# Optimization experiments

Hardware: AMD Instinct MI355X
Metric: run time of the kernel (lower is better)

The kernel has to match this reference:

```python
import jax, jax.numpy as jnp
import numpy as np

B, T, C, H = 8, 2048, 768, 64  # batch, seq_len, embedding_dim, head_size


def setup_inputs() -> dict:
    key = jax.random.key(0)
    k1, k2, k3, k4 = jax.random.split(key, 4)
    x = jax.random.normal(k1, (B, T, C), dtype=jnp.float32)
    attention_mask = jnp.ones((B, T), dtype=jnp.float32)
    # nn.Linear(C, H, bias=False) weights stored pre-transposed as (C, H)
    scale = 0.02
    Wq = jax.random.normal(k2, (C, H), dtype=jnp.float32) * scale
    Wk = jax.random.normal(k3, (C, H), dtype=jnp.float32) * scale
    Wv = jax.random.normal(k4, (C, H), dtype=jnp.float32) * scale
    return {"x": x, "attention_mask": attention_mask, "Wq": Wq, "Wk": Wk, "Wv": Wv}


def reference(x, attention_mask, Wq, Wk, Wv):
    # x: [B,T,C]; attention_mask: [B,T] (multiplied per query row)
    head_size = Wq.shape[-1]
    q = x @ Wq  # [B,T,H]
    k = x @ Wk  # [B,T,H]
    v = x @ Wv  # [B,T,H]
    inv_sqrt_h = jnp.asarray(1.0 / np.sqrt(head_size), x.dtype)
    s = jnp.einsum('bqh,bkh->bqk', q, k) * inv_sqrt_h  # [B,T,T]
    # attention_mask.unsqueeze(2) * qK ; masked_fill(qK == 0, -inf)
    s = attention_mask[:, :, None] * s
    s = jnp.where(s == 0, -jnp.inf, s)
    # causal tril mask
    seq = x.shape[1]
    tril = jnp.tril(jnp.ones((seq, seq), dtype=bool))
    s = jnp.where(tril[None, :, :], s, -jnp.inf)
    p = jax.nn.softmax(s, axis=-1)
    # dropout p=0.0 -> identity; nan cleanup (fully-masked rows)
    p = jnp.where(jnp.isnan(p), jnp.asarray(0.0, p.dtype), p)
    out = jnp.einsum('bqk,bkh->bqh', p, v)  # [B,T,H]
    return out
```

## Files before the change

### kernel.cpp

```cpp
#include <hip/hip_runtime.h>
#include <hip/hip_bf16.h>

#define B_ 8
#define T_ 2048
#define C_ 768
#define H_ 64
#define BT_ (B_*T_)

typedef __attribute__((ext_vector_type(8))) short bf16x8;
typedef __attribute__((ext_vector_type(4))) float f32x4;

__device__ __forceinline__ unsigned short f2bf(float x) {
    __hip_bfloat16 h = __float2bfloat16(x);
    return __builtin_bit_cast(unsigned short, h);
}

__device__ __forceinline__ bf16x8 cvt8(float4 a, float4 b) {
    bf16x8 r;
    r[0] = (short)f2bf(a.x); r[1] = (short)f2bf(a.y);
    r[2] = (short)f2bf(a.z); r[3] = (short)f2bf(a.w);
    r[4] = (short)f2bf(b.x); r[5] = (short)f2bf(b.y);
    r[6] = (short)f2bf(b.z); r[7] = (short)f2bf(b.w);
    return r;
}

__global__ __launch_bounds__(256) void wprep(
    const float* __restrict__ Wq, const float* __restrict__ Wk,
    const float* __restrict__ Wv, unsigned short* __restrict__ WTf)
{
    __shared__ float tile[32][68];
    const int bid = blockIdx.x;
    const int m = bid / 24, gc = bid % 24;
    const float* __restrict__ W = (m == 0) ? Wq : (m == 1) ? Wk : Wv;
    const int t = threadIdx.x;
    {
        const int r = t >> 3, c0 = (t & 7) * 8;
        float4 a = *(const float4*)(W + (size_t)(gc * 32 + r) * H_ + c0);
        float4 b = *(const float4*)(W + (size_t)(gc * 32 + r) * H_ + c0 + 4);
        *(float4*)&tile[r][c0]     = a;
        *(float4*)&tile[r][c0 + 4] = b;
    }
    __syncthreads();
    const int fl = t >> 6, lane = t & 63;
    const int q16 = lane & 15, quad = lane >> 4;
    const int f = m * 4 + fl;
    ushort4 u0, u1;
    u0.x = f2bf(tile[quad * 8 + 0][fl * 16 + q16]);
    u0.y = f2bf(tile[quad * 8 + 1][fl * 16 + q16]);
    u0.z = f2bf(tile[quad * 8 + 2][fl * 16 + q16]);
    u0.w = f2bf(tile[quad * 8 + 3][fl * 16 + q16]);
    u1.x = f2bf(tile[quad * 8 + 4][fl * 16 + q16]);
    u1.y = f2bf(tile[quad * 8 + 5][fl * 16 + q16]);
    u1.z = f2bf(tile[quad * 8 + 6][fl * 16 + q16]);
    u1.w = f2bf(tile[quad * 8 + 7][fl * 16 + q16]);
    unsigned short* __restrict__ dst = WTf + ((size_t)(gc * 12 + f) * 64 + lane) * 8;
    *(ushort4*)(dst)     = u0;
    *(ushort4*)(dst + 4) = u1;
}

__global__ __launch_bounds__(256, 4) void qkv_kernel(
    const float* __restrict__ x, const unsigned short* __restrict__ WTf,
    unsigned short* __restrict__ qF, unsigned short* __restrict__ kF,
    unsigned short* __restrict__ vF)
{
    __shared__ __align__(16) char shraw[3 * 64 * 49 * 4];
    unsigned short* xS = (unsigned short*)shraw;
    float (*mrg)[64][49] = (float (*)[64][49])shraw;

    const int tid  = threadIdx.x;
    const int w    = tid >> 6;
    const int lane = tid & 63;
    const int q16  = lane & 15, quad = lane >> 4;
    const int rowBase = blockIdx.x << 4;

    {
        const int r = tid >> 4, l = tid & 15;
        const float* __restrict__ xrow = x + (size_t)(rowBase + r) * C_;
        #pragma unroll
        for (int i = 0; i < 6; i++) {
            const int j = i * 16 + l;
            float4 a = *(const float4*)(xrow + j * 8);
            float4 b = *(const float4*)(xrow + j * 8 + 4);
            *(bf16x8*)&xS[(size_t)r * 772 + j * 8] = cvt8(a, b);
        }
    }
    __syncthreads();

    const unsigned short* __restrict__ xrowS = xS + q16 * 772 + w * 192 + quad * 8;
    f32x4 acc[12] = {};
    #pragma unroll
    for (int c = 0; c < 6; c++) {
        const int gc = w * 6 + c;
        const unsigned short* __restrict__ wpc = WTf + ((size_t)gc * 12) * 512 + lane * 8;
        bf16x8 xf = *(const bf16x8*)(xrowS + c * 32);
        bf16x8 wf[12];
        #pragma unroll
        for (int f = 0; f < 12; f++)
            wf[f] = *(const bf16x8*)(wpc + f * 512);
        #pragma unroll
        for (int f = 0; f < 12; f++)
            acc[f] = __builtin_amdgcn_mfma_f32_16x16x32_bf16(wf[f], xf, acc[f], 0, 0, 0);
    }
    __syncthreads();

    if (w > 0) {
        #pragma unroll
        for (int f = 0; f < 12; f++)
            #pragma unroll
            for (int r = 0; r < 4; r++) mrg[w - 1][lane][f * 4 + r] = acc[f][r];
    }
    __syncthreads();
    if (w == 0) {
        #pragma unroll
        for (int j = 0; j < 3; j++)
            #pragma unroll
            for (int f = 0; f < 12; f++)
                #pragma unroll
                for (int r = 0; r < 4; r++) acc[f][r] += mrg[j][lane][f * 4 + r];

        const size_t gt = (size_t)(rowBase >> 4);
        #pragma unroll
        for (int f = 0; f < 8; f++) {
            ushort4 u;
            u.x = f2bf(acc[f][0]); u.y = f2bf(acc[f][1]);
            u.z = f2bf(acc[f][2]); u.w = f2bf(acc[f][3]);
            const int n4 = f & 3;
            const int qp = (2 * n4 + (quad >> 1)) & 3;
            const int j0 = (quad & 1) * 4;
            unsigned short* __restrict__ dst = (f < 4) ? qF : kF;
            *(ushort4*)(dst + ((gt * 2 + (n4 >> 1)) * 64 + q16 + 16 * qp) * 8 + j0) = u;
        }
        const size_t g32 = gt >> 1;
        const int qv = ((int)gt & 1) * 2 + (q16 >> 3);
        const int jv = q16 & 7;
        #pragma unroll
        for (int f = 8; f < 12; f++)
            #pragma unroll
            for (int r = 0; r < 4; r++)
                vF[((g32 * 4 + (f - 8)) * 64 + quad * 4 + r + 16 * qv) * 8 + jv] =
                    f2bf(acc[f][r]);
    }
}

__global__ __launch_bounds__(256) void attn_kernel(
    const unsigned short* __restrict__ qF, const unsigned short* __restrict__ kF,
    const unsigned short* __restrict__ vF, const float* __restrict__ mask,
    float* __restrict__ out)
{
    __shared__ __align__(16) unsigned short pS[4][16][88];
    __shared__ float oS[3][64][17];
    __shared__ float mlS[3][64][2];

    const int tid  = threadIdx.x;
    const int w    = tid >> 6;
    const int lane = tid & 63;
    const int q16  = lane & 15;
    const int quad = lane >> 4;
    const int bid  = blockIdx.x;
    const int b    = bid & 7;
    const int qt   = 127 - (bid >> 3);
    const int qrow = (qt << 4) + q16;

    const size_t qbase = ((size_t)(b * 128 + qt) * 2) * 512 + lane * 8;
    bf16x8 qf0 = *(const bf16x8*)(qF + qbase);
    bf16x8 qf1 = *(const bf16x8*)(qF + qbase + 512);
    const float maskv = mask[b * T_ + qrow] * 0.125f * 1.44269504f;

    f32x4 o[4] = {};
    float m_run = -__builtin_inff();
    float l_run = 0.f;

    const int niter = ((qt << 4) + 16 + 63) >> 6;
    for (int kt = w; kt < niter; kt += 4) {
        const int kbase = kt << 6;

        bf16x8 kf[8], vf[8];
        #pragma unroll
        for (int sub = 0; sub < 4; sub++) {
            const unsigned short* kp = kF + ((size_t)(b * 128 + kt * 4 + sub) * 2) * 512 + lane * 8;
            kf[2 * sub]     = *(const bf16x8*)(kp);
            kf[2 * sub + 1] = *(const bf16x8*)(kp + 512);
        }
        #pragma unroll
        for (int ht = 0; ht < 4; ht++) {
            const unsigned short* vp = vF + ((size_t)(b * 64 + kt * 2) * 4 + ht) * 512 + lane * 8;
            vf[2 * ht]     = *(const bf16x8*)(vp);
            vf[2 * ht + 1] = *(const bf16x8*)(vp + 4 * 512);
        }

        f32x4 sa[4] = {};
        #pragma unroll
        for (int sub = 0; sub < 4; sub++) {
            sa[sub] = __builtin_amdgcn_mfma_f32_16x16x32_bf16(kf[2 * sub],     qf0, sa[sub], 0, 0, 0);
            sa[sub] = __builtin_amdgcn_mfma_f32_16x16x32_bf16(kf[2 * sub + 1], qf1, sa[sub], 0, 0, 0);
        }

        float s[16];
        #pragma unroll
        for (int sub = 0; sub < 4; sub++)
            #pragma unroll
            for (int r = 0; r < 4; r++) {
                int kidx = kbase + sub * 16 + quad * 4 + r;
                float sv = sa[sub][r] * maskv;
                sv = (sv == 0.f) ? -__builtin_inff() : sv;
                sv = (kidx > qrow) ? -__builtin_inff() : sv;
                s[sub * 4 + r] = sv;
            }

        float mx = s[0];
        #pragma unroll
        for (int i2 = 1; i2 < 16; i2++) mx = fmaxf(mx, s[i2]);
        mx = fmaxf(mx, __shfl_xor(mx, 16));
        mx = fmaxf(mx, __shfl_xor(mx, 32));
        float m_new = fmaxf(m_run, mx);
        float m_use = (m_new == -__builtin_inff()) ? 0.f : m_new;
        float alpha = exp2f(m_run - m_use);
        float p[16], psum = 0.f;
        #pragma unroll
        for (int i2 = 0; i2 < 16; i2++) { p[i2] = exp2f(s[i2] - m_use); psum += p[i2]; }
        psum += __shfl_xor(psum, 16);
        psum += __shfl_xor(psum, 32);
        l_run = l_run * alpha + psum;
        m_run = m_new;
        #pragma unroll
        for (int ht = 0; ht < 4; ht++)
            #pragma unroll
            for (int r = 0; r < 4; r++) o[ht][r] *= alpha;

        #pragma unroll
        for (int sub = 0; sub < 4; sub++) {
            unsigned int lo = (unsigned int)f2bf(p[sub * 4 + 0]) | ((unsigned int)f2bf(p[sub * 4 + 1]) << 16);
            unsigned int hi = (unsigned int)f2bf(p[sub * 4 + 2]) | ((unsigned int)f2bf(p[sub * 4 + 3]) << 16);
            *(uint2*)&pS[w][q16][sub * 16 + quad * 4] = make_uint2(lo, hi);
        }
        bf16x8 pf0 = *(const bf16x8*)&pS[w][q16][quad * 8];
        bf16x8 pf1 = *(const bf16x8*)&pS[w][q16][32 + quad * 8];

        #pragma unroll
        for (int ht = 0; ht < 4; ht++) {
            o[ht] = __builtin_amdgcn_mfma_f32_16x16x32_bf16(vf[2 * ht],     pf0, o[ht], 0, 0, 0);
            o[ht] = __builtin_amdgcn_mfma_f32_16x16x32_bf16(vf[2 * ht + 1], pf1, o[ht], 0, 0, 0);
        }
    }

    if (w > 0) {
        mlS[w - 1][lane][0] = m_run;
        mlS[w - 1][lane][1] = l_run;
        #pragma unroll
        for (int ht = 0; ht < 4; ht++)
            #pragma unroll
            for (int r = 0; r < 4; r++) oS[w - 1][lane][ht * 4 + r] = o[ht][r];
    }
    __syncthreads();
    if (w == 0) {
        float mm[3], ll[3];
        float m = m_run;
        #pragma unroll
        for (int j = 0; j < 3; j++) {
            mm[j] = mlS[j][lane][0]; ll[j] = mlS[j][lane][1];
            m = fmaxf(m, mm[j]);
        }
        float mu = (m == -__builtin_inff()) ? 0.f : m;
        float a0 = exp2f(m_run - mu);
        float aj[3];
        float l = l_run * a0;
        #pragma unroll
        for (int j = 0; j < 3; j++) { aj[j] = exp2f(mm[j] - mu); l += ll[j] * aj[j]; }
        float invl = (l > 0.f) ? (1.f / l) : 0.f;
        #pragma unroll
        for (int ht = 0; ht < 4; ht++) {
            float4 ov;
            float vx = o[ht][0] * a0, vy = o[ht][1] * a0, vz = o[ht][2] * a0, vw2 = o[ht][3] * a0;
            #pragma unroll
            for (int j = 0; j < 3; j++) {
                vx += oS[j][lane][ht * 4 + 0] * aj[j];
                vy += oS[j][lane][ht * 4 + 1] * aj[j];
                vz += oS[j][lane][ht * 4 + 2] * aj[j];
                vw2 += oS[j][lane][ht * 4 + 3] * aj[j];
            }
            ov.x = vx * invl; ov.y = vy * invl; ov.z = vz * invl; ov.w = vw2 * invl;
            *(float4*)(out + ((size_t)(b * T_) + qrow) * H_ + ht * 16 + quad * 4) = ov;
        }
    }
}

extern "C" void kernel_launch(void* const* d_in, const int* in_sizes, int n_in,
                              void* d_out, int out_size, void* d_ws, size_t ws_size,
                              hipStream_t stream) {
    const float* x    = (const float*)d_in[0];
    const float* mask = (const float*)d_in[1];
    const float* Wq   = (const float*)d_in[2];
    const float* Wk   = (const float*)d_in[3];
    const float* Wv   = (const float*)d_in[4];
    float* out = (float*)d_out;

    unsigned short* qf = (unsigned short*)d_ws;
    unsigned short* kf = qf + (size_t)BT_ * H_;
    unsigned short* vf = kf + (size_t)BT_ * H_;
    unsigned short* wt = vf + (size_t)BT_ * H_;

    wprep<<<72, 256, 0, stream>>>(Wq, Wk, Wv, wt);
    qkv_kernel<<<BT_ / 16, 256, 0, stream>>>(x, wt, qf, kf, vf);
    attn_kernel<<<B_ * (T_ / 16), 256, 0, stream>>>(qf, kf, vf, mask, out);
}
```

Measured before the change: 118.1 us.

## Split QKV projection across waves by output fragment instead of K-chunks

Each wave now owns 3 of the 12 output fragments and loops over the full K dimension (24 chunks), instead of each wave computing all 12 fragments over a quarter of K and then merging partials through shared memory. This removes the LDS reduction buffer, two barriers and the serial epilogue on wave 0, and cuts accumulator registers from 12 to 3 vectors. In exchange, each wave runs a longer dependent MFMA chain with fewer independent accumulators, and every wave reads the whole x row tile from LDS. The occupancy hint in launch bounds is dropped.

```diff
diff --git a/kernel.cpp b/kernel.cpp
--- a/kernel.cpp
+++ b/kernel.cpp
@@ -58,15 +58,12 @@
     *(ushort4*)(dst + 4) = u1;
 }
 
-__global__ __launch_bounds__(256, 4) void qkv_kernel(
+__global__ __launch_bounds__(256) void qkv_kernel(
     const float* __restrict__ x, const unsigned short* __restrict__ WTf,
     unsigned short* __restrict__ qF, unsigned short* __restrict__ kF,
     unsigned short* __restrict__ vF)
 {
-    __shared__ __align__(16) char shraw[3 * 64 * 49 * 4];
-    unsigned short* xS = (unsigned short*)shraw;
-    float (*mrg)[64][49] = (float (*)[64][49])shraw;
-
+    __shared__ __align__(16) unsigned short xS[16 * 772];
     const int tid  = threadIdx.x;
     const int w    = tid >> 6;
     const int lane = tid & 63;
@@ -86,59 +83,44 @@
     }
     __syncthreads();
 
-    const unsigned short* __restrict__ xrowS = xS + q16 * 772 + w * 192 + quad * 8;
-    f32x4 acc[12] = {};
+    const int f0 = w * 3;
+    const unsigned short* __restrict__ xrowS = xS + q16 * 772 + quad * 8;
+    f32x4 acc[3] = {};
     #pragma unroll
-    for (int c = 0; c < 6; c++) {
-        const int gc = w * 6 + c;
-        const unsigned short* __restrict__ wpc = WTf + ((size_t)gc * 12) * 512 + lane * 8;
+    for (int c = 0; c < 24; c++) {
+        const unsigned short* __restrict__ wpc =
+            WTf + ((size_t)(c * 12 + f0)) * 512 + lane * 8;
         bf16x8 xf = *(const bf16x8*)(xrowS + c * 32);
-        bf16x8 wf[12];
-        #pragma unroll
-        for (int f = 0; f < 12; f++)
-            wf[f] = *(const bf16x8*)(wpc + f * 512);
-        #pragma unroll
-        for (int f = 0; f < 12; f++)
-            acc[f] = __builtin_amdgcn_mfma_f32_16x16x32_bf16(wf[f], xf, acc[f], 0, 0, 0);
-    }
-    __syncthreads();
-
-    if (w > 0) {
-        #pragma unroll
-        for (int f = 0; f < 12; f++)
-            #pragma unroll
-            for (int r = 0; r < 4; r++) mrg[w - 1][lane][f * 4 + r] = acc[f][r];
-    }
-    __syncthreads();
-    if (w == 0) {
-        #pragma unroll
-        for (int j = 0; j < 3; j++)
-            #pragma unroll
-            for (int f = 0; f < 12; f++)
-                #pragma unroll
-                for (int r = 0; r < 4; r++) acc[f][r] += mrg[j][lane][f * 4 + r];
-
-        const size_t gt = (size_t)(rowBase >> 4);
-        #pragma unroll
-        for (int f = 0; f < 8; f++) {
+        bf16x8 w0 = *(const bf16x8*)(wpc);
+        bf16x8 w1 = *(const bf16x8*)(wpc + 512);
+        bf16x8 w2 = *(const bf16x8*)(wpc + 1024);
+        acc[0] = __builtin_amdgcn_mfma_f32_16x16x32_bf16(w0, xf, acc[0], 0, 0, 0);
+        acc[1] = __builtin_amdgcn_mfma_f32_16x16x32_bf16(w1, xf, acc[1], 0, 0, 0);
+        acc[2] = __builtin_amdgcn_mfma_f32_16x16x32_bf16(w2, xf, acc[2], 0, 0, 0);
+    }
+
+    const size_t gt = (size_t)(rowBase >> 4);
+    #pragma unroll
+    for (int j = 0; j < 3; j++) {
+        const int f = f0 + j;
+        if (f < 8) {
             ushort4 u;
-            u.x = f2bf(acc[f][0]); u.y = f2bf(acc[f][1]);
-            u.z = f2bf(acc[f][2]); u.w = f2bf(acc[f][3]);
+            u.x = f2bf(acc[j][0]); u.y = f2bf(acc[j][1]);
+            u.z = f2bf(acc[j][2]); u.w = f2bf(acc[j][3]);
             const int n4 = f & 3;
             const int qp = (2 * n4 + (quad >> 1)) & 3;
             const int j0 = (quad & 1) * 4;
             unsigned short* __restrict__ dst = (f < 4) ? qF : kF;
             *(ushort4*)(dst + ((gt * 2 + (n4 >> 1)) * 64 + q16 + 16 * qp) * 8 + j0) = u;
-        }
-        const size_t g32 = gt >> 1;
-        const int qv = ((int)gt & 1) * 2 + (q16 >> 3);
-        const int jv = q16 & 7;
-        #pragma unroll
-        for (int f = 8; f < 12; f++)
+        } else {
+            const size_t g32 = gt >> 1;
+            const int qv = ((int)gt & 1) * 2 + (q16 >> 3);
+            const int jv = q16 & 7;
             #pragma unroll
             for (int r = 0; r < 4; r++)
                 vF[((g32 * 4 + (f - 8)) * 64 + quad * 4 + r + 16 * qv) * 8 + jv] =
-                    f2bf(acc[f][r]);
+                    f2bf(acc[j][r]);
+        }
     }
 }
 
```

After: 118.6 us. No clear change (+0.4%).
